# Optimization experiments

Measured on AMD Instinct MI355X. Metric: run time of the kernel, lower is better.

Reference implementation:

```python
import jax, jax.numpy as jnp
import numpy as np

BATCH = 8
N_CLASSES = 3            # including background
PRE_NMS_LIMIT = 6000
NMS_THRESH = 0.5
SCALE = 512.0
WINDOW = (0.0, 0.0, 512.0, 512.0)   # y1, x1, y2, x2
STD_DEV = np.array([0.1, 0.1, 0.2, 0.2], np.float32)
GROUP_OFFSET = 4096.0    # > image extent; separates (batch, class) groups in NMS

_RATIOS = np.array([0.5, 1.0, 2.0])
_LEVELS = [((128, 128), 4, 8.0), ((64, 64), 8, 16.0), ((32, 32), 16, 32.0), ((16, 16), 32, 64.0)]


def _gen_anchors():
    # faithful port of generate_pyramid_anchors / generate_anchors (anchor_stride=1)
    out = []
    for (fy, fx), stride, scale in _LEVELS:
        s, r = np.meshgrid(np.array([scale]), _RATIOS)
        s, r = s.flatten(), r.flatten()
        heights = s / np.sqrt(r)
        widths = s * np.sqrt(r)
        sy = np.arange(fy) * stride
        sx = np.arange(fx) * stride
        sx, sy = np.meshgrid(sx, sy)
        bw, bcx = np.meshgrid(widths, sx)
        bh, bcy = np.meshgrid(heights, sy)
        centers = np.stack([bcy, bcx], axis=2).reshape(-1, 2)
        sizes = np.stack([bh, bw], axis=2).reshape(-1, 2)
        out.append(np.concatenate([centers - 0.5 * sizes, centers + 0.5 * sizes], axis=1))
    return np.concatenate(out, axis=0).astype(np.float32)  # (65280, 4) yxyx


def setup_inputs() -> dict:
    key = jax.random.key(0)
    k1, k2 = jax.random.split(key)
    anchors = jnp.asarray(_gen_anchors())
    n_anchors = anchors.shape[0]
    n_prop = BATCH * n_anchors
    logits = jax.random.normal(k1, (n_prop, N_CLASSES), jnp.float32)
    probs = jax.nn.softmax(logits, axis=-1)
    deltas = jax.random.normal(k2, (n_prop, 4), jnp.float32)
    batch_ixs = jnp.repeat(jnp.arange(BATCH, dtype=jnp.int64), n_anchors)
    return {"probs": probs, "deltas": deltas, "anchors": anchors, "batch_ixs": batch_ixs}


def _apply_box_deltas_2d(boxes, deltas):
    # boxes: (K,4) yxyx (normalized); deltas: (K,4) dy,dx,dh,dw
    h = boxes[:, 2] - boxes[:, 0]
    w = boxes[:, 3] - boxes[:, 1]
    cy = boxes[:, 0] + 0.5 * h + deltas[:, 0] * h
    cx = boxes[:, 1] + 0.5 * w + deltas[:, 1] * w
    h = h * jnp.exp(deltas[:, 2])
    w = w * jnp.exp(deltas[:, 3])
    y1 = cy - 0.5 * h
    x1 = cx - 0.5 * w
    return jnp.stack([y1, x1, y1 + h, x1 + w], axis=1)


def _nms_keep(boxes, thresh):
    # boxes (K,4), already sorted by score descending; returns bool keep mask.
    y1, x1, y2, x2 = boxes[:, 0], boxes[:, 1], boxes[:, 2], boxes[:, 3]
    areas = (y2 - y1 + 1.0) * (x2 - x1 + 1.0)
    ih = jnp.clip(jnp.minimum(y2[:, None], y2[None, :]) - jnp.maximum(y1[:, None], y1[None, :]) + 1.0, 0.0)
    iw = jnp.clip(jnp.minimum(x2[:, None], x2[None, :]) - jnp.maximum(x1[:, None], x1[None, :]) + 1.0, 0.0)
    inter = ih * iw
    iou = inter / (areas[:, None] + areas[None, :] - inter)  # (K,K)
    K = boxes.shape[0]
    idx = jnp.arange(K)

    def body(i, keep):
        sup = (iou[i] >= thresh) & (idx > i) & keep[i]
        return keep & ~sup

    return jax.lax.fori_loop(0, K, body, jnp.ones((K,), bool))


def reference(probs, deltas, anchors, batch_ixs):
    n_anchors = anchors.shape[0]
    n_fg = probs.shape[1] - 1
    # trim to top pre_nms_limit foreground scores (flat over proposals x fg classes)
    fg = probs[:, 1:].reshape(-1)
    scores, flat_ix = jax.lax.top_k(fg, PRE_NMS_LIMIT)  # sorted descending
    prop_ix = flat_ix // n_fg
    class_ids = flat_ix % n_fg + 1
    b = batch_ixs[prop_ix]
    a = anchors[prop_ix % n_anchors]        # anchors tiled per batch element
    d = deltas[prop_ix] * jnp.asarray(STD_DEV)
    rois = _apply_box_deltas_2d(a / SCALE, d) * SCALE
    lo = jnp.array([WINDOW[0], WINDOW[1], WINDOW[0], WINDOW[1]], rois.dtype)
    hi = jnp.array([WINDOW[2], WINDOW[3], WINDOW[2], WINDOW[3]], rois.dtype)
    rois = jnp.clip(rois, lo, hi)
    # batched per-class NMS: offset boxes so different (batch, class) groups never overlap
    group = (b * (n_fg + 1) + class_ids).astype(rois.dtype) * GROUP_OFFSET
    keep = _nms_keep(rois + group[:, None], NMS_THRESH)
    detections = jnp.concatenate(
        [rois, scores[:, None], keep.astype(rois.dtype)[:, None]], axis=1)  # (K, 6)
    return detections, class_ids, b
```

## Files before the change

kernel.cpp:

```cpp
#include <hip/hip_runtime.h>
#include <math.h>

typedef unsigned int u32;
typedef unsigned short u16;
typedef unsigned long long u64;

#define PRE_NMS 6000
#define NBLK    94
#define KMAX    640
#define MSTRIDE 11
#define MAXW    10
#define MTILE   (MAXW * MAXW)
#define FINEB   8192
#define LOWB    8064
#define TOTB    (FINEB + LOWB)
#define NHB     16
#define CANDMAX 16384
#define SLICES  8
#define NGRP    24
#define CBLK    256
#define CBUF    512
#define FLOOR_BITS 0x3F000000u

#define CTR_OFF    0
#define RANKS_OFF  256
#define PART_OFF   65792
#define CAND_OFF   1106176
#define BOXR_OFF   1237248
#define GBITS_OFF  1333504
#define KG_OFF     1351936
#define GRANKG_OFF 1352192
#define BOXG_OFF   1413632
#define AREAG_OFF  1659392
#define MASKG_OFF  1720832

__global__ __launch_bounds__(1024) void hist_kernel(const float4* __restrict__ probs4,
                                                    u32* __restrict__ partials, int n_prop) {
    __shared__ u32 hf[FINEB];
    __shared__ u32 hl[2][LOWB];
    int t = threadIdx.x;
    for (int i = t; i < FINEB; i += 1024) hf[i] = 0u;
    for (int i = t; i < 2 * LOWB; i += 1024) ((u32*)hl)[i] = 0u;
    __syncthreads();
    u32* l = hl[(t >> 6) & 1];
    int nq = n_prop >> 2;
    int idx = blockIdx.x * 1024 + t;
    int stride = gridDim.x * 1024;
    for (int q = idx; q < nq; q += stride) {
        float4 a = probs4[3 * q + 0];
        float4 b = probs4[3 * q + 1];
        float4 c = probs4[3 * q + 2];
        float vs[8] = {a.y, a.z, b.x, b.y, b.w, c.x, c.z, c.w};
        #pragma unroll
        for (int e = 0; e < 8; ++e) {
            u32 bits = __float_as_uint(vs[e]);
            if (bits >= FLOOR_BITS) {
                u32 fb = (bits - FLOOR_BITS) >> 10; if (fb >= FINEB) fb = FINEB - 1;
                atomicAdd(&hf[fb], 1u);
            } else {
                atomicAdd(&l[bits >> 17], 1u);
            }
        }
    }
    __syncthreads();
    u32* outp = partials + blockIdx.x * TOTB;
    for (int b = t; b < FINEB; b += 1024) outp[b] = hf[b];
    for (int b = t; b < LOWB; b += 1024) outp[FINEB + b] = hl[0][b] + hl[1][b];
}

__global__ __launch_bounds__(1024) void pivot_kernel(const u32* __restrict__ partials,
                                                     u32* __restrict__ ctr,
                                                     u32* __restrict__ ranks,
                                                     u32* __restrict__ gbits) {
    __shared__ u32 fh[FINEB];
    __shared__ u32 sd[1024];
    int t = threadIdx.x;
    for (int i = t; i < CANDMAX; i += 1024) ranks[i] = 0u;
    for (int i = t; i < NGRP * 192; i += 1024) gbits[i] = 0u;
    if (t == 0) ctr[0] = 0u;
    for (int b = t; b < FINEB; b += 1024) {
        u32 s = 0;
        #pragma unroll
        for (int k = 0; k < NHB; ++k) s += partials[k * TOTB + b];
        fh[b] = s;
    }
    __syncthreads();
    int hi = FINEB - 1 - 8 * t;
    u32 L = 0;
    #pragma unroll
    for (int e = 0; e < 8; ++e) L += fh[hi - e];
    sd[t] = L;
    __syncthreads();
    for (int off = 1; off < 1024; off <<= 1) {
        u32 x = (t >= off) ? sd[t - off] : 0u;
        __syncthreads();
        sd[t] += x;
        __syncthreads();
    }
    u32 incl = sd[t], excl = incl - L;
    u32 fineTotal = sd[1023];
    if (excl < (u32)PRE_NMS && incl >= (u32)PRE_NMS) {
        u32 run = excl;
        #pragma unroll
        for (int e = 0; e < 8; ++e) {
            u32 c = fh[hi - e];
            if (run < (u32)PRE_NMS && run + c >= (u32)PRE_NMS)
                ctr[1] = FLOOR_BITS + ((u32)(hi - e) << 10);
            run += c;
        }
    }
    if (fineTotal >= (u32)PRE_NMS) return;

    u32 rem = (u32)PRE_NMS - fineTotal;
    __syncthreads();
    for (int b = t; b < FINEB; b += 1024) {
        u32 s = 0;
        if (b < LOWB) {
            #pragma unroll
            for (int k = 0; k < NHB; ++k) s += partials[k * TOTB + FINEB + b];
        }
        fh[b] = s;
    }
    __syncthreads();
    L = 0;
    #pragma unroll
    for (int e = 0; e < 8; ++e) L += fh[hi - e];
    sd[t] = L;
    __syncthreads();
    for (int off = 1; off < 1024; off <<= 1) {
        u32 x = (t >= off) ? sd[t - off] : 0u;
        __syncthreads();
        sd[t] += x;
        __syncthreads();
    }
    incl = sd[t]; excl = incl - L;
    if (excl < rem && incl >= rem) {
        u32 run = excl;
        #pragma unroll
        for (int e = 0; e < 8; ++e) {
            u32 c = fh[hi - e];
            if (run < rem && run + c >= rem)
                ctr[1] = ((u32)(hi - e)) << 17;
            run += c;
        }
    }
}

__global__ __launch_bounds__(256) void compact_kernel(const float4* __restrict__ probs4,
                                                      u32* ctr, u64* __restrict__ cand,
                                                      int n_prop) {
    __shared__ u64 sloc[CBUF];
    __shared__ u32 scnt, sbase;
    int t = threadIdx.x;
    if (t == 0) scnt = 0u;
    __syncthreads();
    u32 pivot = ctr[1];
    int nq = n_prop >> 2;
    int idx = blockIdx.x * 256 + t;
    int stride = gridDim.x * 256;
    for (int q = idx; q < nq; q += stride) {
        float4 a = probs4[3 * q + 0];
        float4 b = probs4[3 * q + 1];
        float4 c = probs4[3 * q + 2];
        float vs[8] = {a.y, a.z, b.x, b.y, b.w, c.x, c.z, c.w};
        #pragma unroll
        for (int e = 0; e < 8; ++e) {
            u32 bits = __float_as_uint(vs[e]);
            if (bits >= pivot) {
                u32 lp = atomicAdd(&scnt, 1u);
                u32 i = (u32)(8 * q + e);
                if (lp < (u32)CBUF) sloc[lp] = ((u64)bits << 32) | (u64)(~i);
            }
        }
    }
    __syncthreads();
    u32 cnt = scnt; if (cnt > (u32)CBUF) cnt = (u32)CBUF;
    if (t == 0) sbase = atomicAdd(&ctr[0], cnt);
    __syncthreads();
    u32 base = sbase;
    for (u32 j = t; j < cnt; j += 256) {
        u32 pos = base + j;
        if (pos < (u32)CANDMAX) cand[pos] = sloc[j];
    }
}

__global__ __launch_bounds__(256) void rank_kernel(const u64* __restrict__ cand,
                                                   const u32* __restrict__ ctr,
                                                   u32* __restrict__ ranks) {
    __shared__ u64 tile[256];
    int t = threadIdx.x;
    u32 M = ctr[0]; if (M > (u32)CANDMAX) M = (u32)CANDMAX;
    int kb = blockIdx.y;
    if ((u32)(kb * 256) >= M) return;
    int i = kb * 256 + t;
    u64 key = (i < (int)M) ? cand[i] : 0ull;
    u32 Ls = (M + SLICES - 1) / SLICES;
    u32 s0 = blockIdx.x * Ls;
    u32 s1 = s0 + Ls; if (s1 > M) s1 = M;
    int cnt = 0;
    for (u32 base = s0; base < s1; base += 256) {
        u32 idx = base + t;
        tile[t] = (idx < s1) ? cand[idx] : 0ull;
        __syncthreads();
        #pragma unroll 8
        for (int q = 0; q < 256; ++q) cnt += (tile[q] > key) ? 1 : 0;
        __syncthreads();
    }
    if (i < (int)M && cnt > 0) atomicAdd(&ranks[i], (u32)cnt);
}

__global__ __launch_bounds__(256) void decode_kernel(const u64* __restrict__ cand,
                                                     const u32* __restrict__ ranks,
                                                     const u32* __restrict__ ctr,
                                                     const float4* __restrict__ deltas4,
                                                     const float4* __restrict__ anchors4,
                                                     float4* __restrict__ boxr,
                                                     u32* __restrict__ gbits,
                                                     float* __restrict__ out,
                                                     int n_anch) {
    u32 i = blockIdx.x * 256 + threadIdx.x;
    u32 M = ctr[0]; if (M > (u32)CANDMAX) M = (u32)CANDMAX;
    if (i >= M) return;
    u32 r = ranks[i];
    if (r >= (u32)PRE_NMS) return;
    u64 key = cand[i];
    u32 bits = (u32)(key >> 32);
    u32 flat = ~((u32)key);
    int p = (int)(flat >> 1);
    int cls = (int)(flat & 1u) + 1;
    int b = p / n_anch;
    int g = b * 3 + cls;
    int aidx = p - b * n_anch;
    float score = __uint_as_float(bits);
    float4 a = anchors4[aidx];
    float4 d = deltas4[p];
    float d0 = d.x * 0.1f, d1 = d.y * 0.1f, d2 = d.z * 0.2f, d3 = d.w * 0.2f;
    float y1 = a.x * (1.0f / 512.0f), x1 = a.y * (1.0f / 512.0f);
    float y2 = a.z * (1.0f / 512.0f), x2 = a.w * (1.0f / 512.0f);
    float h = y2 - y1, w = x2 - x1;
    float cy = y1 + 0.5f * h + d0 * h;
    float cx = x1 + 0.5f * w + d1 * w;
    h = h * expf(d2);
    w = w * expf(d3);
    float ry1 = (cy - 0.5f * h) * 512.0f;
    float rx1 = (cx - 0.5f * w) * 512.0f;
    float ry2 = (cy - 0.5f * h + h) * 512.0f;
    float rx2 = (cx - 0.5f * w + w) * 512.0f;
    ry1 = fminf(fmaxf(ry1, 0.0f), 512.0f);
    rx1 = fminf(fmaxf(rx1, 0.0f), 512.0f);
    ry2 = fminf(fmaxf(ry2, 0.0f), 512.0f);
    rx2 = fminf(fmaxf(rx2, 0.0f), 512.0f);
    out[r * 6 + 0] = ry1;
    out[r * 6 + 1] = rx1;
    out[r * 6 + 2] = ry2;
    out[r * 6 + 3] = rx2;
    out[r * 6 + 4] = score;
    out[r * 6 + 5] = 1.0f;
    out[PRE_NMS * 6 + r] = (float)cls;
    out[PRE_NMS * 7 + r] = (float)b;
    boxr[r] = make_float4(ry1, rx1, ry2, rx2);
    atomicOr(&gbits[g * 192 + (r >> 5)], 1u << (r & 31));
}

__global__ __launch_bounds__(512) void prep_kernel(const u32* __restrict__ gbits,
                                                   const float4* __restrict__ boxr,
                                                   u32* __restrict__ kg,
                                                   u32* __restrict__ grankg,
                                                   float4* __restrict__ boxg,
                                                   float* __restrict__ areag) {
    __shared__ int bpre[96];
    __shared__ u16 grankS[KMAX];
    __shared__ int sK;
    int g = blockIdx.x, t = threadIdx.x, lane = t & 63, wv = t >> 6;
    const u32* rb32 = gbits + g * 192;

    if (t < 64) {
        u64 w0 = (u64)rb32[2 * lane] | ((u64)rb32[2 * lane + 1] << 32);
        u64 w1 = (lane < NBLK - 64)
                 ? ((u64)rb32[128 + 2 * lane] | ((u64)rb32[129 + 2 * lane] << 32)) : 0ull;
        int c0 = (int)__popcll(w0), c1 = (int)__popcll(w1);
        int i0 = c0, i1 = c1;
        #pragma unroll
        for (int off = 1; off < 64; off <<= 1) {
            int a = __shfl_up(i0, off); if (lane >= off) i0 += a;
            int b = __shfl_up(i1, off); if (lane >= off) i1 += b;
        }
        int tot0 = __shfl(i0, 63), tot1 = __shfl(i1, 63);
        bpre[lane] = i0 - c0;
        if (lane < 32) bpre[64 + lane] = tot0 + ((lane < NBLK - 64) ? (i1 - c1) : 0);
        if (lane == 0) { sK = tot0 + tot1; kg[g] = (u32)(tot0 + tot1); }
    }
    __syncthreads();
    int K = sK;
    if (K == 0) return;
    int Kc = (K < KMAX) ? K : KMAX;

    for (int blk = wv; blk < NBLK; blk += 8) {
        u64 wmask = (u64)rb32[2 * blk] | ((u64)rb32[2 * blk + 1] << 32);
        if ((wmask >> lane) & 1ull) {
            int pos = bpre[blk] + (int)__popcll(wmask & ((1ull << lane) - 1ull));
            if (pos < KMAX) grankS[pos] = (u16)((blk << 6) | lane);
        }
    }
    __syncthreads();

    float4* bg = boxg + g * KMAX;
    float*  ag = areag + g * KMAX;
    u32*    gr = grankg + g * KMAX;
    for (int m = t; m < KMAX; m += 512) {
        if (m < Kc) {
            int r = grankS[m];
            float4 bb = boxr[r];
            bg[m] = bb;
            ag[m] = (bb.z - bb.x + 1.0f) * (bb.w - bb.y + 1.0f);
            gr[m] = (u32)r;
        } else {
            bg[m] = make_float4(-3e30f, -3e30f, -3e30f, -3e30f);
            ag[m] = 3e38f;
        }
    }
}

__global__ __launch_bounds__(64) void mask_kernel(const u32* __restrict__ kg,
                                                  const float4* __restrict__ boxg,
                                                  const float* __restrict__ areag,
                                                  u64* __restrict__ maskg) {
    int g = blockIdx.y;
    u32 K = kg[g];
    if (K == 0u) return;
    int Kc = (K < (u32)KMAX) ? (int)K : KMAX;
    int W = (Kc + 63) >> 6;
    int u = blockIdx.x;
    int c = u / MAXW, rbk = u % MAXW;
    if (c >= W || rbk >= W) return;
    int lane = threadIdx.x;
    int r = rbk * 64 + lane;
    u64* mg = maskg + (size_t)g * (KMAX * MSTRIDE);
    if (rbk > c) { mg[r * MSTRIDE + c] = 0ull; return; }
    int j0 = c << 6;
    const float4* bg = boxg + g * KMAX;
    const float*  ag = areag + g * KMAX;
    float4 rb = bg[r];
    float  ra = ag[r];
    float4 cb = bg[j0 + lane];
    float  ca = ag[j0 + lane];
    u64 word = 0ull;
    #pragma unroll 8
    for (int q = 0; q < 64; ++q) {
        float cbx = __shfl(cb.x, q);
        float cby = __shfl(cb.y, q);
        float cbz = __shfl(cb.z, q);
        float cbw = __shfl(cb.w, q);
        float cav = __shfl(ca, q);
        float ih = fminf(rb.z, cbz) - fmaxf(rb.x, cbx) + 1.0f;
        float iw = fminf(rb.w, cbw) - fmaxf(rb.y, cby) + 1.0f;
        ih = fmaxf(ih, 0.0f); iw = fmaxf(iw, 0.0f);
        bool o = (3.0f * ih * iw >= ra + cav) && ((j0 + q) > r);
        if (o) word |= (1ull << q);
    }
    mg[r * MSTRIDE + c] = word;
}

__global__ __launch_bounds__(512) void greedy_kernel(const u32* __restrict__ kg,
                                                     const u32* __restrict__ grankg,
                                                     const u64* __restrict__ maskg,
                                                     float* __restrict__ out) {
    __shared__ u64 maskm[KMAX * MSTRIDE + 64];
    __shared__ u16 grank[KMAX];
    int g = blockIdx.x, t = threadIdx.x, lane = t & 63;
    u32 K = kg[g];
    if (K == 0u) return;
    int Kc = (K < (u32)KMAX) ? (int)K : KMAX;
    int W = (Kc + 63) >> 6;
    const u64* mg = maskg + (size_t)g * (KMAX * MSTRIDE);
    int nw = Kc * MSTRIDE;
    for (int m = t; m < nw; m += 512) maskm[m] = mg[m];
    for (int m = nw + t; m < nw + 64; m += 512) maskm[m] = 0ull;
    for (int m = t; m < Kc; m += 512) grank[m] = (u16)grankg[g * KMAX + m];
    __syncthreads();

    if (t >= 64) return;
    u64 remv = 0ull;
    for (int w = 0; w < W; ++w) {
        int r0 = w << 6;
        int rend = Kc - r0; if (rend > 64) rend = 64;
        u64 curw = __shfl(remv, w);
        u64 kb = 0ull;
        for (int b0 = 0; b0 < rend; b0 += 8) {
            int n = rend - b0; if (n > 8) n = 8;
            u64 mrow[8], dg[8];
            #pragma unroll
            for (int j = 0; j < 8; ++j) {
                int rr = r0 + b0 + ((j < n) ? j : 0);
                mrow[j] = maskm[rr * MSTRIDE + lane];
                dg[j]   = maskm[rr * MSTRIDE + w];
            }
            #pragma unroll
            for (int j = 0; j < 8; ++j) {
                if (j < n) {
                    int b = b0 + j;
                    u64 km = ((curw >> b) & 1ull) ? 0ull : ~0ull;
                    curw |= dg[j] & km;
                    remv |= mrow[j] & km;
                    kb |= km & (1ull << b);
                }
            }
        }
        if (lane < rend)
            out[(int)grank[r0 + lane] * 6 + 5] = ((kb >> lane) & 1ull) ? 1.0f : 0.0f;
    }
}

extern "C" void kernel_launch(void* const* d_in, const int* in_sizes, int n_in,
                              void* d_out, int out_size, void* d_ws, size_t ws_size,
                              hipStream_t stream) {
    const float*  probs    = (const float*)d_in[0];
    const float4* deltas4  = (const float4*)d_in[1];
    const float4* anchors4 = (const float4*)d_in[2];
    int n_prop = in_sizes[1] / 4;
    int n_anch = in_sizes[2] / 4;

    char* ws = (char*)d_ws;
    u32* ctr      = (u32*)(ws + CTR_OFF);
    u32* ranks    = (u32*)(ws + RANKS_OFF);
    u32* partials = (u32*)(ws + PART_OFF);
    u64* cand     = (u64*)(ws + CAND_OFF);
    float4* boxr  = (float4*)(ws + BOXR_OFF);
    u32* gbits    = (u32*)(ws + GBITS_OFF);
    u32* kg       = (u32*)(ws + KG_OFF);
    u32* grankg   = (u32*)(ws + GRANKG_OFF);
    float4* boxg  = (float4*)(ws + BOXG_OFF);
    float* areag  = (float*)(ws + AREAG_OFF);
    u64* maskg    = (u64*)(ws + MASKG_OFF);
    float* out    = (float*)d_out;

    hist_kernel<<<NHB, 1024, 0, stream>>>((const float4*)probs, partials, n_prop);
    pivot_kernel<<<1, 1024, 0, stream>>>(partials, ctr, ranks, gbits);
    compact_kernel<<<CBLK, 256, 0, stream>>>((const float4*)probs, ctr, cand, n_prop);
    rank_kernel<<<dim3(SLICES, 64), 256, 0, stream>>>(cand, ctr, ranks);
    decode_kernel<<<CANDMAX / 256, 256, 0, stream>>>(cand, ranks, ctr, deltas4, anchors4,
                                                     boxr, gbits, out, n_anch);
    prep_kernel<<<NGRP, 512, 0, stream>>>(gbits, boxr, kg, grankg, boxg, areag);
    mask_kernel<<<dim3(MTILE, NGRP), 64, 0, stream>>>(kg, boxg, areag, maskg);
    greedy_kernel<<<NGRP, 512, 0, stream>>>(kg, grankg, maskg, out);
}
```

Baseline: 153.5 us.

## Fuse the eight-kernel pipeline into one cooperative kernel with grid syncs

Replaces the eight separate launches (hist, pivot, compact, rank, decode, prep, mask, greedy) with a single cooperative mega-kernel of 256 blocks separated by grid.sync barriers. The aim is to remove launch overhead and the gaps between dependent stages. The histogram now runs on all 256 blocks, with global atomics into a shared fine histogram and per-block low partials. The rank and compact phases are also reworked inside the fused kernel. In exchange, the single-block pivot phase now has to sum 256 low partials instead of 16. The grid-wide barriers have their own cost, and the large shared-memory pool limits occupancy to one block per CU.

```diff
diff --git a/kernel.cpp b/kernel.cpp
--- a/kernel.cpp
+++ b/kernel.cpp
@@ -1,5 +1,8 @@
 #include <hip/hip_runtime.h>
+#include <hip/hip_cooperative_groups.h>
 #include <math.h>
+
+namespace cg = cooperative_groups;
 
 typedef unsigned int u32;
 typedef unsigned short u16;
@@ -10,437 +13,410 @@
 #define KMAX    640
 #define MSTRIDE 11
 #define MAXW    10
-#define MTILE   (MAXW * MAXW)
 #define FINEB   8192
 #define LOWB    8064
-#define TOTB    (FINEB + LOWB)
-#define NHB     16
 #define CANDMAX 16384
-#define SLICES  8
 #define NGRP    24
-#define CBLK    256
 #define CBUF    512
+#define NBLOCKS 256
+#define NTHREADS 256
+#define NTOT    (NBLOCKS * NTHREADS)
 #define FLOOR_BITS 0x3F000000u
 
 #define CTR_OFF    0
-#define RANKS_OFF  256
-#define PART_OFF   65792
-#define CAND_OFF   1106176
-#define BOXR_OFF   1237248
-#define GBITS_OFF  1333504
-#define KG_OFF     1351936
-#define GRANKG_OFF 1352192
-#define BOXG_OFF   1413632
-#define AREAG_OFF  1659392
-#define MASKG_OFF  1720832
-
-__global__ __launch_bounds__(1024) void hist_kernel(const float4* __restrict__ probs4,
-                                                    u32* __restrict__ partials, int n_prop) {
-    __shared__ u32 hf[FINEB];
-    __shared__ u32 hl[2][LOWB];
-    int t = threadIdx.x;
-    for (int i = t; i < FINEB; i += 1024) hf[i] = 0u;
-    for (int i = t; i < 2 * LOWB; i += 1024) ((u32*)hl)[i] = 0u;
-    __syncthreads();
-    u32* l = hl[(t >> 6) & 1];
-    int nq = n_prop >> 2;
-    int idx = blockIdx.x * 1024 + t;
-    int stride = gridDim.x * 1024;
-    for (int q = idx; q < nq; q += stride) {
-        float4 a = probs4[3 * q + 0];
-        float4 b = probs4[3 * q + 1];
-        float4 c = probs4[3 * q + 2];
-        float vs[8] = {a.y, a.z, b.x, b.y, b.w, c.x, c.z, c.w};
+#define CAND_OFF   256
+#define BOXR_OFF   131328
+#define GBITS_OFF  227584
+#define KG_OFF     246016
+#define GRANKG_OFF 246272
+#define BOXG_OFF   307712
+#define AREAG_OFF  553472
+#define MASKG_OFF  614912
+#define FINEH_OFF  1966592
+#define LOWP_OFF   1999360
+
+__global__ __launch_bounds__(NTHREADS) void mega_kernel(
+    const float4* __restrict__ probs4,
+    const float4* __restrict__ deltas4,
+    const float4* __restrict__ anchors4,
+    float* __restrict__ out,
+    char* __restrict__ ws,
+    int n_prop, int n_anch)
+{
+    cg::grid_group grid = cg::this_grid();
+
+    u32*    ctr    = (u32*)(ws + CTR_OFF);
+    u64*    cand   = (u64*)(ws + CAND_OFF);
+    float4* boxr   = (float4*)(ws + BOXR_OFF);
+    u32*    gbits  = (u32*)(ws + GBITS_OFF);
+    u32*    kg     = (u32*)(ws + KG_OFF);
+    u32*    grankg = (u32*)(ws + GRANKG_OFF);
+    float4* boxg   = (float4*)(ws + BOXG_OFF);
+    float*  areag  = (float*)(ws + AREAG_OFF);
+    u64*    maskg  = (u64*)(ws + MASKG_OFF);
+    u32*    fineh  = (u32*)(ws + FINEH_OFF);
+    u32*    lowp   = (u32*)(ws + LOWP_OFF);
+
+    __shared__ __align__(16) unsigned char pool[65024];
+    __shared__ u32 s_cnt, s_base;
+    __shared__ int s_K;
+
+    const int t    = threadIdx.x;
+    const int bid  = blockIdx.x;
+    const int gtid = bid * NTHREADS + t;
+    const int lane = t & 63, wv = t >> 6;
+
+    for (int i = gtid; i < FINEB; i += NTOT) fineh[i] = 0u;
+    if (gtid < 64) ctr[gtid] = 0u;
+    for (int i = gtid; i < NGRP * 192; i += NTOT) gbits[i] = 0u;
+    grid.sync();
+
+    {
+        u32* hf = (u32*)pool;
+        u32* hl = hf + FINEB;
+        for (int i = t; i < FINEB + LOWB; i += NTHREADS) hf[i] = 0u;
+        __syncthreads();
+        int nq = n_prop >> 2;
+        for (int q = gtid; q < nq; q += NTOT) {
+            float4 a = probs4[3 * q + 0];
+            float4 b = probs4[3 * q + 1];
+            float4 c = probs4[3 * q + 2];
+            float vs[8] = {a.y, a.z, b.x, b.y, b.w, c.x, c.z, c.w};
+            #pragma unroll
+            for (int e = 0; e < 8; ++e) {
+                u32 bits = __float_as_uint(vs[e]);
+                if (bits >= FLOOR_BITS) {
+                    u32 fb = (bits - FLOOR_BITS) >> 10; if (fb >= FINEB) fb = FINEB - 1;
+                    atomicAdd(&hf[fb], 1u);
+                } else {
+                    atomicAdd(&hl[bits >> 17], 1u);
+                }
+            }
+        }
+        __syncthreads();
+        for (int i = t; i < FINEB; i += NTHREADS) {
+            u32 v = hf[i];
+            if (v) atomicAdd(&fineh[i], v);
+        }
+        u32* myLow = lowp + bid * LOWB;
+        for (int i = t; i < LOWB; i += NTHREADS) myLow[i] = hl[i];
+    }
+    grid.sync();
+
+    if (bid == 0) {
+        u32* fh = (u32*)pool;
+        u32* sd = fh + FINEB;
+        for (int b = t; b < FINEB; b += NTHREADS) fh[b] = fineh[b];
+        __syncthreads();
+        int hi = FINEB - 1 - 32 * t;
+        u32 L = 0;
         #pragma unroll
-        for (int e = 0; e < 8; ++e) {
-            u32 bits = __float_as_uint(vs[e]);
-            if (bits >= FLOOR_BITS) {
-                u32 fb = (bits - FLOOR_BITS) >> 10; if (fb >= FINEB) fb = FINEB - 1;
-                atomicAdd(&hf[fb], 1u);
-            } else {
-                atomicAdd(&l[bits >> 17], 1u);
-            }
-        }
-    }
-    __syncthreads();
-    u32* outp = partials + blockIdx.x * TOTB;
-    for (int b = t; b < FINEB; b += 1024) outp[b] = hf[b];
-    for (int b = t; b < LOWB; b += 1024) outp[FINEB + b] = hl[0][b] + hl[1][b];
-}
-
-__global__ __launch_bounds__(1024) void pivot_kernel(const u32* __restrict__ partials,
-                                                     u32* __restrict__ ctr,
-                                                     u32* __restrict__ ranks,
-                                                     u32* __restrict__ gbits) {
-    __shared__ u32 fh[FINEB];
-    __shared__ u32 sd[1024];
-    int t = threadIdx.x;
-    for (int i = t; i < CANDMAX; i += 1024) ranks[i] = 0u;
-    for (int i = t; i < NGRP * 192; i += 1024) gbits[i] = 0u;
-    if (t == 0) ctr[0] = 0u;
-    for (int b = t; b < FINEB; b += 1024) {
-        u32 s = 0;
-        #pragma unroll
-        for (int k = 0; k < NHB; ++k) s += partials[k * TOTB + b];
-        fh[b] = s;
-    }
-    __syncthreads();
-    int hi = FINEB - 1 - 8 * t;
-    u32 L = 0;
-    #pragma unroll
-    for (int e = 0; e < 8; ++e) L += fh[hi - e];
-    sd[t] = L;
-    __syncthreads();
-    for (int off = 1; off < 1024; off <<= 1) {
-        u32 x = (t >= off) ? sd[t - off] : 0u;
-        __syncthreads();
-        sd[t] += x;
-        __syncthreads();
-    }
-    u32 incl = sd[t], excl = incl - L;
-    u32 fineTotal = sd[1023];
-    if (excl < (u32)PRE_NMS && incl >= (u32)PRE_NMS) {
-        u32 run = excl;
-        #pragma unroll
-        for (int e = 0; e < 8; ++e) {
-            u32 c = fh[hi - e];
-            if (run < (u32)PRE_NMS && run + c >= (u32)PRE_NMS)
-                ctr[1] = FLOOR_BITS + ((u32)(hi - e) << 10);
-            run += c;
-        }
-    }
-    if (fineTotal >= (u32)PRE_NMS) return;
-
-    u32 rem = (u32)PRE_NMS - fineTotal;
-    __syncthreads();
-    for (int b = t; b < FINEB; b += 1024) {
-        u32 s = 0;
-        if (b < LOWB) {
+        for (int e = 0; e < 32; ++e) L += fh[hi - e];
+        sd[t] = L;
+        __syncthreads();
+        for (int off = 1; off < NTHREADS; off <<= 1) {
+            u32 x = (t >= off) ? sd[t - off] : 0u;
+            __syncthreads();
+            sd[t] += x;
+            __syncthreads();
+        }
+        u32 incl = sd[t], excl = incl - L;
+        u32 fineTotal = sd[NTHREADS - 1];
+        if (excl < (u32)PRE_NMS && incl >= (u32)PRE_NMS) {
+            u32 run = excl;
+            for (int e = 0; e < 32; ++e) {
+                u32 c = fh[hi - e];
+                if (run < (u32)PRE_NMS && run + c >= (u32)PRE_NMS)
+                    ctr[1] = FLOOR_BITS + ((u32)(hi - e) << 10);
+                run += c;
+            }
+        }
+        if (fineTotal < (u32)PRE_NMS) {
+            u32 rem = (u32)PRE_NMS - fineTotal;
+            __syncthreads();
+            for (int b = t; b < FINEB; b += NTHREADS) {
+                u32 s = 0;
+                if (b < LOWB) {
+                    for (int k = 0; k < NBLOCKS; ++k) s += lowp[k * LOWB + b];
+                }
+                fh[b] = s;
+            }
+            __syncthreads();
+            L = 0;
+            for (int e = 0; e < 32; ++e) L += fh[hi - e];
+            sd[t] = L;
+            __syncthreads();
+            for (int off = 1; off < NTHREADS; off <<= 1) {
+                u32 x = (t >= off) ? sd[t - off] : 0u;
+                __syncthreads();
+                sd[t] += x;
+                __syncthreads();
+            }
+            incl = sd[t]; excl = incl - L;
+            if (excl < rem && incl >= rem) {
+                u32 run = excl;
+                for (int e = 0; e < 32; ++e) {
+                    u32 c = fh[hi - e];
+                    if (run < rem && run + c >= rem)
+                        ctr[1] = ((u32)(hi - e)) << 17;
+                    run += c;
+                }
+            }
+        }
+    }
+    grid.sync();
+
+    {
+        u64* sloc = (u64*)pool;
+        if (t == 0) s_cnt = 0u;
+        __syncthreads();
+        u32 pivot = ctr[1];
+        int nq = n_prop >> 2;
+        for (int q = gtid; q < nq; q += NTOT) {
+            float4 a = probs4[3 * q + 0];
+            float4 b = probs4[3 * q + 1];
+            float4 c = probs4[3 * q + 2];
+            float vs[8] = {a.y, a.z, b.x, b.y, b.w, c.x, c.z, c.w};
             #pragma unroll
-            for (int k = 0; k < NHB; ++k) s += partials[k * TOTB + FINEB + b];
-        }
-        fh[b] = s;
-    }
-    __syncthreads();
-    L = 0;
-    #pragma unroll
-    for (int e = 0; e < 8; ++e) L += fh[hi - e];
-    sd[t] = L;
-    __syncthreads();
-    for (int off = 1; off < 1024; off <<= 1) {
-        u32 x = (t >= off) ? sd[t - off] : 0u;
-        __syncthreads();
-        sd[t] += x;
-        __syncthreads();
-    }
-    incl = sd[t]; excl = incl - L;
-    if (excl < rem && incl >= rem) {
-        u32 run = excl;
-        #pragma unroll
-        for (int e = 0; e < 8; ++e) {
-            u32 c = fh[hi - e];
-            if (run < rem && run + c >= rem)
-                ctr[1] = ((u32)(hi - e)) << 17;
-            run += c;
-        }
-    }
-}
-
-__global__ __launch_bounds__(256) void compact_kernel(const float4* __restrict__ probs4,
-                                                      u32* ctr, u64* __restrict__ cand,
-                                                      int n_prop) {
-    __shared__ u64 sloc[CBUF];
-    __shared__ u32 scnt, sbase;
-    int t = threadIdx.x;
-    if (t == 0) scnt = 0u;
-    __syncthreads();
-    u32 pivot = ctr[1];
-    int nq = n_prop >> 2;
-    int idx = blockIdx.x * 256 + t;
-    int stride = gridDim.x * 256;
-    for (int q = idx; q < nq; q += stride) {
-        float4 a = probs4[3 * q + 0];
-        float4 b = probs4[3 * q + 1];
-        float4 c = probs4[3 * q + 2];
-        float vs[8] = {a.y, a.z, b.x, b.y, b.w, c.x, c.z, c.w};
-        #pragma unroll
-        for (int e = 0; e < 8; ++e) {
-            u32 bits = __float_as_uint(vs[e]);
-            if (bits >= pivot) {
-                u32 lp = atomicAdd(&scnt, 1u);
-                u32 i = (u32)(8 * q + e);
-                if (lp < (u32)CBUF) sloc[lp] = ((u64)bits << 32) | (u64)(~i);
-            }
-        }
-    }
-    __syncthreads();
-    u32 cnt = scnt; if (cnt > (u32)CBUF) cnt = (u32)CBUF;
-    if (t == 0) sbase = atomicAdd(&ctr[0], cnt);
-    __syncthreads();
-    u32 base = sbase;
-    for (u32 j = t; j < cnt; j += 256) {
-        u32 pos = base + j;
-        if (pos < (u32)CANDMAX) cand[pos] = sloc[j];
-    }
-}
-
-__global__ __launch_bounds__(256) void rank_kernel(const u64* __restrict__ cand,
-                                                   const u32* __restrict__ ctr,
-                                                   u32* __restrict__ ranks) {
-    __shared__ u64 tile[256];
-    int t = threadIdx.x;
-    u32 M = ctr[0]; if (M > (u32)CANDMAX) M = (u32)CANDMAX;
-    int kb = blockIdx.y;
-    if ((u32)(kb * 256) >= M) return;
-    int i = kb * 256 + t;
-    u64 key = (i < (int)M) ? cand[i] : 0ull;
-    u32 Ls = (M + SLICES - 1) / SLICES;
-    u32 s0 = blockIdx.x * Ls;
-    u32 s1 = s0 + Ls; if (s1 > M) s1 = M;
-    int cnt = 0;
-    for (u32 base = s0; base < s1; base += 256) {
-        u32 idx = base + t;
-        tile[t] = (idx < s1) ? cand[idx] : 0ull;
-        __syncthreads();
-        #pragma unroll 8
-        for (int q = 0; q < 256; ++q) cnt += (tile[q] > key) ? 1 : 0;
-        __syncthreads();
-    }
-    if (i < (int)M && cnt > 0) atomicAdd(&ranks[i], (u32)cnt);
-}
-
-__global__ __launch_bounds__(256) void decode_kernel(const u64* __restrict__ cand,
-                                                     const u32* __restrict__ ranks,
-                                                     const u32* __restrict__ ctr,
-                                                     const float4* __restrict__ deltas4,
-                                                     const float4* __restrict__ anchors4,
-                                                     float4* __restrict__ boxr,
-                                                     u32* __restrict__ gbits,
-                                                     float* __restrict__ out,
-                                                     int n_anch) {
-    u32 i = blockIdx.x * 256 + threadIdx.x;
-    u32 M = ctr[0]; if (M > (u32)CANDMAX) M = (u32)CANDMAX;
-    if (i >= M) return;
-    u32 r = ranks[i];
-    if (r >= (u32)PRE_NMS) return;
-    u64 key = cand[i];
-    u32 bits = (u32)(key >> 32);
-    u32 flat = ~((u32)key);
-    int p = (int)(flat >> 1);
-    int cls = (int)(flat & 1u) + 1;
-    int b = p / n_anch;
-    int g = b * 3 + cls;
-    int aidx = p - b * n_anch;
-    float score = __uint_as_float(bits);
-    float4 a = anchors4[aidx];
-    float4 d = deltas4[p];
-    float d0 = d.x * 0.1f, d1 = d.y * 0.1f, d2 = d.z * 0.2f, d3 = d.w * 0.2f;
-    float y1 = a.x * (1.0f / 512.0f), x1 = a.y * (1.0f / 512.0f);
-    float y2 = a.z * (1.0f / 512.0f), x2 = a.w * (1.0f / 512.0f);
-    float h = y2 - y1, w = x2 - x1;
-    float cy = y1 + 0.5f * h + d0 * h;
-    float cx = x1 + 0.5f * w + d1 * w;
-    h = h * expf(d2);
-    w = w * expf(d3);
-    float ry1 = (cy - 0.5f * h) * 512.0f;
-    float rx1 = (cx - 0.5f * w) * 512.0f;
-    float ry2 = (cy - 0.5f * h + h) * 512.0f;
-    float rx2 = (cx - 0.5f * w + w) * 512.0f;
-    ry1 = fminf(fmaxf(ry1, 0.0f), 512.0f);
-    rx1 = fminf(fmaxf(rx1, 0.0f), 512.0f);
-    ry2 = fminf(fmaxf(ry2, 0.0f), 512.0f);
-    rx2 = fminf(fmaxf(rx2, 0.0f), 512.0f);
-    out[r * 6 + 0] = ry1;
-    out[r * 6 + 1] = rx1;
-    out[r * 6 + 2] = ry2;
-    out[r * 6 + 3] = rx2;
-    out[r * 6 + 4] = score;
-    out[r * 6 + 5] = 1.0f;
-    out[PRE_NMS * 6 + r] = (float)cls;
-    out[PRE_NMS * 7 + r] = (float)b;
-    boxr[r] = make_float4(ry1, rx1, ry2, rx2);
-    atomicOr(&gbits[g * 192 + (r >> 5)], 1u << (r & 31));
-}
-
-__global__ __launch_bounds__(512) void prep_kernel(const u32* __restrict__ gbits,
-                                                   const float4* __restrict__ boxr,
-                                                   u32* __restrict__ kg,
-                                                   u32* __restrict__ grankg,
-                                                   float4* __restrict__ boxg,
-                                                   float* __restrict__ areag) {
-    __shared__ int bpre[96];
-    __shared__ u16 grankS[KMAX];
-    __shared__ int sK;
-    int g = blockIdx.x, t = threadIdx.x, lane = t & 63, wv = t >> 6;
-    const u32* rb32 = gbits + g * 192;
-
-    if (t < 64) {
-        u64 w0 = (u64)rb32[2 * lane] | ((u64)rb32[2 * lane + 1] << 32);
-        u64 w1 = (lane < NBLK - 64)
-                 ? ((u64)rb32[128 + 2 * lane] | ((u64)rb32[129 + 2 * lane] << 32)) : 0ull;
-        int c0 = (int)__popcll(w0), c1 = (int)__popcll(w1);
-        int i0 = c0, i1 = c1;
-        #pragma unroll
-        for (int off = 1; off < 64; off <<= 1) {
-            int a = __shfl_up(i0, off); if (lane >= off) i0 += a;
-            int b = __shfl_up(i1, off); if (lane >= off) i1 += b;
-        }
-        int tot0 = __shfl(i0, 63), tot1 = __shfl(i1, 63);
-        bpre[lane] = i0 - c0;
-        if (lane < 32) bpre[64 + lane] = tot0 + ((lane < NBLK - 64) ? (i1 - c1) : 0);
-        if (lane == 0) { sK = tot0 + tot1; kg[g] = (u32)(tot0 + tot1); }
-    }
-    __syncthreads();
-    int K = sK;
-    if (K == 0) return;
-    int Kc = (K < KMAX) ? K : KMAX;
-
-    for (int blk = wv; blk < NBLK; blk += 8) {
-        u64 wmask = (u64)rb32[2 * blk] | ((u64)rb32[2 * blk + 1] << 32);
-        if ((wmask >> lane) & 1ull) {
-            int pos = bpre[blk] + (int)__popcll(wmask & ((1ull << lane) - 1ull));
-            if (pos < KMAX) grankS[pos] = (u16)((blk << 6) | lane);
-        }
-    }
-    __syncthreads();
-
-    float4* bg = boxg + g * KMAX;
-    float*  ag = areag + g * KMAX;
-    u32*    gr = grankg + g * KMAX;
-    for (int m = t; m < KMAX; m += 512) {
-        if (m < Kc) {
-            int r = grankS[m];
-            float4 bb = boxr[r];
-            bg[m] = bb;
-            ag[m] = (bb.z - bb.x + 1.0f) * (bb.w - bb.y + 1.0f);
-            gr[m] = (u32)r;
-        } else {
-            bg[m] = make_float4(-3e30f, -3e30f, -3e30f, -3e30f);
-            ag[m] = 3e38f;
-        }
-    }
-}
-
-__global__ __launch_bounds__(64) void mask_kernel(const u32* __restrict__ kg,
-                                                  const float4* __restrict__ boxg,
-                                                  const float* __restrict__ areag,
-                                                  u64* __restrict__ maskg) {
-    int g = blockIdx.y;
-    u32 K = kg[g];
-    if (K == 0u) return;
-    int Kc = (K < (u32)KMAX) ? (int)K : KMAX;
-    int W = (Kc + 63) >> 6;
-    int u = blockIdx.x;
-    int c = u / MAXW, rbk = u % MAXW;
-    if (c >= W || rbk >= W) return;
-    int lane = threadIdx.x;
-    int r = rbk * 64 + lane;
-    u64* mg = maskg + (size_t)g * (KMAX * MSTRIDE);
-    if (rbk > c) { mg[r * MSTRIDE + c] = 0ull; return; }
-    int j0 = c << 6;
-    const float4* bg = boxg + g * KMAX;
-    const float*  ag = areag + g * KMAX;
-    float4 rb = bg[r];
-    float  ra = ag[r];
-    float4 cb = bg[j0 + lane];
-    float  ca = ag[j0 + lane];
-    u64 word = 0ull;
-    #pragma unroll 8
-    for (int q = 0; q < 64; ++q) {
-        float cbx = __shfl(cb.x, q);
-        float cby = __shfl(cb.y, q);
-        float cbz = __shfl(cb.z, q);
-        float cbw = __shfl(cb.w, q);
-        float cav = __shfl(ca, q);
-        float ih = fminf(rb.z, cbz) - fmaxf(rb.x, cbx) + 1.0f;
-        float iw = fminf(rb.w, cbw) - fmaxf(rb.y, cby) + 1.0f;
-        ih = fmaxf(ih, 0.0f); iw = fmaxf(iw, 0.0f);
-        bool o = (3.0f * ih * iw >= ra + cav) && ((j0 + q) > r);
-        if (o) word |= (1ull << q);
-    }
-    mg[r * MSTRIDE + c] = word;
-}
-
-__global__ __launch_bounds__(512) void greedy_kernel(const u32* __restrict__ kg,
-                                                     const u32* __restrict__ grankg,
-                                                     const u64* __restrict__ maskg,
-                                                     float* __restrict__ out) {
-    __shared__ u64 maskm[KMAX * MSTRIDE + 64];
-    __shared__ u16 grank[KMAX];
-    int g = blockIdx.x, t = threadIdx.x, lane = t & 63;
-    u32 K = kg[g];
-    if (K == 0u) return;
-    int Kc = (K < (u32)KMAX) ? (int)K : KMAX;
-    int W = (Kc + 63) >> 6;
-    const u64* mg = maskg + (size_t)g * (KMAX * MSTRIDE);
-    int nw = Kc * MSTRIDE;
-    for (int m = t; m < nw; m += 512) maskm[m] = mg[m];
-    for (int m = nw + t; m < nw + 64; m += 512) maskm[m] = 0ull;
-    for (int m = t; m < Kc; m += 512) grank[m] = (u16)grankg[g * KMAX + m];
-    __syncthreads();
-
-    if (t >= 64) return;
-    u64 remv = 0ull;
-    for (int w = 0; w < W; ++w) {
-        int r0 = w << 6;
-        int rend = Kc - r0; if (rend > 64) rend = 64;
-        u64 curw = __shfl(remv, w);
-        u64 kb = 0ull;
-        for (int b0 = 0; b0 < rend; b0 += 8) {
-            int n = rend - b0; if (n > 8) n = 8;
-            u64 mrow[8], dg[8];
-            #pragma unroll
-            for (int j = 0; j < 8; ++j) {
-                int rr = r0 + b0 + ((j < n) ? j : 0);
-                mrow[j] = maskm[rr * MSTRIDE + lane];
-                dg[j]   = maskm[rr * MSTRIDE + w];
-            }
-            #pragma unroll
-            for (int j = 0; j < 8; ++j) {
-                if (j < n) {
-                    int b = b0 + j;
-                    u64 km = ((curw >> b) & 1ull) ? 0ull : ~0ull;
-                    curw |= dg[j] & km;
-                    remv |= mrow[j] & km;
-                    kb |= km & (1ull << b);
-                }
-            }
-        }
-        if (lane < rend)
-            out[(int)grank[r0 + lane] * 6 + 5] = ((kb >> lane) & 1ull) ? 1.0f : 0.0f;
+            for (int e = 0; e < 8; ++e) {
+                u32 bits = __float_as_uint(vs[e]);
+                if (bits >= pivot) {
+                    u32 lp = atomicAdd(&s_cnt, 1u);
+                    u32 i = (u32)(8 * q + e);
+                    if (lp < (u32)CBUF) sloc[lp] = ((u64)bits << 32) | (u64)(~i);
+                }
+            }
+        }
+        __syncthreads();
+        u32 cnt = s_cnt; if (cnt > (u32)CBUF) cnt = (u32)CBUF;
+        if (t == 0) s_base = atomicAdd(&ctr[0], cnt);
+        __syncthreads();
+        for (u32 j = t; j < cnt; j += NTHREADS) {
+            u32 pos = s_base + j;
+            if (pos < (u32)CANDMAX) cand[pos] = sloc[j];
+        }
+    }
+    grid.sync();
+
+    {
+        u64* tile = (u64*)pool;
+        u32 M = ctr[0]; if (M > (u32)CANDMAX) M = (u32)CANDMAX;
+        u32 i = (u32)gtid;
+        u64 key = (i < M) ? cand[i] : 0ull;
+        u32 cnt = 0;
+        for (u32 base = 0; base < M; base += 2048) {
+            for (u32 j = t; j < 2048; j += NTHREADS) {
+                u32 idx = base + j;
+                tile[j] = (idx < M) ? cand[idx] : 0ull;
+            }
+            __syncthreads();
+            #pragma unroll 8
+            for (int q = 0; q < 2048; ++q) cnt += (tile[q] > key) ? 1u : 0u;
+            __syncthreads();
+        }
+        if (i < M && cnt < (u32)PRE_NMS) {
+            u32 r = cnt;
+            u32 bits = (u32)(key >> 32);
+            u32 flat = ~((u32)key);
+            int p = (int)(flat >> 1);
+            int cls = (int)(flat & 1u) + 1;
+            int b = p / n_anch;
+            int g = b * 3 + cls;
+            int aidx = p - b * n_anch;
+            float score = __uint_as_float(bits);
+            float4 a = anchors4[aidx];
+            float4 d = deltas4[p];
+            float d0 = d.x * 0.1f, d1 = d.y * 0.1f, d2 = d.z * 0.2f, d3 = d.w * 0.2f;
+            float y1 = a.x * (1.0f / 512.0f), x1 = a.y * (1.0f / 512.0f);
+            float y2 = a.z * (1.0f / 512.0f), x2 = a.w * (1.0f / 512.0f);
+            float h = y2 - y1, w = x2 - x1;
+            float cy = y1 + 0.5f * h + d0 * h;
+            float cx = x1 + 0.5f * w + d1 * w;
+            h = h * expf(d2);
+            w = w * expf(d3);
+            float ry1 = (cy - 0.5f * h) * 512.0f;
+            float rx1 = (cx - 0.5f * w) * 512.0f;
+            float ry2 = (cy - 0.5f * h + h) * 512.0f;
+            float rx2 = (cx - 0.5f * w + w) * 512.0f;
+            ry1 = fminf(fmaxf(ry1, 0.0f), 512.0f);
+            rx1 = fminf(fmaxf(rx1, 0.0f), 512.0f);
+            ry2 = fminf(fmaxf(ry2, 0.0f), 512.0f);
+            rx2 = fminf(fmaxf(rx2, 0.0f), 512.0f);
+            out[r * 6 + 0] = ry1;
+            out[r * 6 + 1] = rx1;
+            out[r * 6 + 2] = ry2;
+            out[r * 6 + 3] = rx2;
+            out[r * 6 + 4] = score;
+            out[r * 6 + 5] = 1.0f;
+            out[PRE_NMS * 6 + r] = (float)cls;
+            out[PRE_NMS * 7 + r] = (float)b;
+            boxr[r] = make_float4(ry1, rx1, ry2, rx2);
+            atomicOr(&gbits[g * 192 + (r >> 5)], 1u << (r & 31));
+        }
+    }
+    grid.sync();
+
+    {
+        int* bpre   = (int*)pool;
+        u16* grankS = (u16*)(pool + 512);
+        int g = bid;
+        if (g < NGRP) {
+            const u32* rb32 = gbits + g * 192;
+            if (t < 64) {
+                u64 w0 = (u64)rb32[2 * lane] | ((u64)rb32[2 * lane + 1] << 32);
+                u64 w1 = (lane < NBLK - 64)
+                         ? ((u64)rb32[128 + 2 * lane] | ((u64)rb32[129 + 2 * lane] << 32)) : 0ull;
+                int c0 = (int)__popcll(w0), c1 = (int)__popcll(w1);
+                int i0 = c0, i1 = c1;
+                #pragma unroll
+                for (int off = 1; off < 64; off <<= 1) {
+                    int a = __shfl_up(i0, off); if (lane >= off) i0 += a;
+                    int b = __shfl_up(i1, off); if (lane >= off) i1 += b;
+                }
+                int tot0 = __shfl(i0, 63), tot1 = __shfl(i1, 63);
+                bpre[lane] = i0 - c0;
+                if (lane < 32) bpre[64 + lane] = tot0 + ((lane < NBLK - 64) ? (i1 - c1) : 0);
+                if (lane == 0) { s_K = tot0 + tot1; kg[g] = (u32)(tot0 + tot1); }
+            }
+            __syncthreads();
+            int K = s_K;
+            if (K > 0) {
+                int Kc = (K < KMAX) ? K : KMAX;
+                for (int blk = wv; blk < NBLK; blk += 4) {
+                    u64 wmask = (u64)rb32[2 * blk] | ((u64)rb32[2 * blk + 1] << 32);
+                    if ((wmask >> lane) & 1ull) {
+                        int pos = bpre[blk] + (int)__popcll(wmask & ((1ull << lane) - 1ull));
+                        if (pos < KMAX) grankS[pos] = (u16)((blk << 6) | lane);
+                    }
+                }
+                __syncthreads();
+                float4* bg = boxg + g * KMAX;
+                float*  ag = areag + g * KMAX;
+                u32*    gr = grankg + g * KMAX;
+                for (int m = t; m < KMAX; m += NTHREADS) {
+                    if (m < Kc) {
+                        int r = grankS[m];
+                        float4 bb = boxr[r];
+                        bg[m] = bb;
+                        ag[m] = (bb.z - bb.x + 1.0f) * (bb.w - bb.y + 1.0f);
+                        gr[m] = (u32)r;
+                    } else {
+                        bg[m] = make_float4(-3e30f, -3e30f, -3e30f, -3e30f);
+                        ag[m] = 3e38f;
+                    }
+                }
+            }
+        }
+    }
+    grid.sync();
+
+    {
+        int gw = bid * 4 + wv;
+        const int NUNIT = NGRP * MAXW * MAXW;
+        for (int u = gw; u < NUNIT; u += NBLOCKS * 4) {
+            int g = u / (MAXW * MAXW);
+            int rm = u % (MAXW * MAXW);
+            int c = rm / MAXW, rbk = rm % MAXW;
+            u32 K = kg[g];
+            if (K == 0u) continue;
+            int Kc = (K < (u32)KMAX) ? (int)K : KMAX;
+            int W = (Kc + 63) >> 6;
+            if (c >= W || rbk >= W) continue;
+            int r = rbk * 64 + lane;
+            u64* mg = maskg + (size_t)g * (KMAX * MSTRIDE);
+            if (rbk > c) { mg[r * MSTRIDE + c] = 0ull; continue; }
+            int j0 = c << 6;
+            const float4* bg = boxg + g * KMAX;
+            const float*  ag = areag + g * KMAX;
+            float4 rb = bg[r];
+            float  ra = ag[r];
+            float4 cb = bg[j0 + lane];
+            float  ca = ag[j0 + lane];
+            u64 word = 0ull;
+            #pragma unroll 8
+            for (int q = 0; q < 64; ++q) {
+                float cbx = __shfl(cb.x, q);
+                float cby = __shfl(cb.y, q);
+                float cbz = __shfl(cb.z, q);
+                float cbw = __shfl(cb.w, q);
+                float cav = __shfl(ca, q);
+                float ih = fminf(rb.z, cbz) - fmaxf(rb.x, cbx) + 1.0f;
+                float iw = fminf(rb.w, cbw) - fmaxf(rb.y, cby) + 1.0f;
+                ih = fmaxf(ih, 0.0f); iw = fmaxf(iw, 0.0f);
+                bool o = (3.0f * ih * iw >= ra + cav) && ((j0 + q) > r);
+                if (o) word |= (1ull << q);
+            }
+            mg[r * MSTRIDE + c] = word;
+        }
+    }
+    grid.sync();
+
+    {
+        int g = bid;
+        if (g < NGRP) {
+            u32 K = kg[g];
+            if (K > 0u) {
+                u64* maskm = (u64*)pool;
+                u16* grank = (u16*)(pool + 57344);
+                int Kc = (K < (u32)KMAX) ? (int)K : KMAX;
+                int W = (Kc + 63) >> 6;
+                const u64* mg = maskg + (size_t)g * (KMAX * MSTRIDE);
+                int nw = Kc * MSTRIDE;
+                for (int m = t; m < nw; m += NTHREADS) maskm[m] = mg[m];
+                for (int m = nw + t; m < nw + 64; m += NTHREADS) maskm[m] = 0ull;
+                for (int m = t; m < Kc; m += NTHREADS) grank[m] = (u16)grankg[g * KMAX + m];
+                __syncthreads();
+                if (t < 64) {
+                    u64 remv = 0ull;
+                    for (int w = 0; w < W; ++w) {
+                        int r0 = w << 6;
+                        int rend = Kc - r0; if (rend > 64) rend = 64;
+                        u64 curw = __shfl(remv, w);
+                        u64 kb = 0ull;
+                        for (int b0 = 0; b0 < rend; b0 += 8) {
+                            int n = rend - b0; if (n > 8) n = 8;
+                            u64 mrow[8], dg[8];
+                            #pragma unroll
+                            for (int j = 0; j < 8; ++j) {
+                                int rr = r0 + b0 + ((j < n) ? j : 0);
+                                mrow[j] = maskm[rr * MSTRIDE + lane];
+                                dg[j]   = maskm[rr * MSTRIDE + w];
+                            }
+                            #pragma unroll
+                            for (int j = 0; j < 8; ++j) {
+                                if (j < n) {
+                                    int b = b0 + j;
+                                    u64 km = ((curw >> b) & 1ull) ? 0ull : ~0ull;
+                                    curw |= dg[j] & km;
+                                    remv |= mrow[j] & km;
+                                    kb |= km & (1ull << b);
+                                }
+                            }
+                        }
+                        if (lane < rend)
+                            out[(int)grank[r0 + lane] * 6 + 5] = ((kb >> lane) & 1ull) ? 1.0f : 0.0f;
+                    }
+                }
+            }
+        }
     }
 }
 
 extern "C" void kernel_launch(void* const* d_in, const int* in_sizes, int n_in,
                               void* d_out, int out_size, void* d_ws, size_t ws_size,
                               hipStream_t stream) {
-    const float*  probs    = (const float*)d_in[0];
+    const float4* probs4   = (const float4*)d_in[0];
     const float4* deltas4  = (const float4*)d_in[1];
     const float4* anchors4 = (const float4*)d_in[2];
     int n_prop = in_sizes[1] / 4;
     int n_anch = in_sizes[2] / 4;
-
-    char* ws = (char*)d_ws;
-    u32* ctr      = (u32*)(ws + CTR_OFF);
-    u32* ranks    = (u32*)(ws + RANKS_OFF);
-    u32* partials = (u32*)(ws + PART_OFF);
-    u64* cand     = (u64*)(ws + CAND_OFF);
-    float4* boxr  = (float4*)(ws + BOXR_OFF);
-    u32* gbits    = (u32*)(ws + GBITS_OFF);
-    u32* kg       = (u32*)(ws + KG_OFF);
-    u32* grankg   = (u32*)(ws + GRANKG_OFF);
-    float4* boxg  = (float4*)(ws + BOXG_OFF);
-    float* areag  = (float*)(ws + AREAG_OFF);
-    u64* maskg    = (u64*)(ws + MASKG_OFF);
-    float* out    = (float*)d_out;
-
-    hist_kernel<<<NHB, 1024, 0, stream>>>((const float4*)probs, partials, n_prop);
-    pivot_kernel<<<1, 1024, 0, stream>>>(partials, ctr, ranks, gbits);
-    compact_kernel<<<CBLK, 256, 0, stream>>>((const float4*)probs, ctr, cand, n_prop);
-    rank_kernel<<<dim3(SLICES, 64), 256, 0, stream>>>(cand, ctr, ranks);
-    decode_kernel<<<CANDMAX / 256, 256, 0, stream>>>(cand, ranks, ctr, deltas4, anchors4,
-                                                     boxr, gbits, out, n_anch);
-    prep_kernel<<<NGRP, 512, 0, stream>>>(gbits, boxr, kg, grankg, boxg, areag);
-    mask_kernel<<<dim3(MTILE, NGRP), 64, 0, stream>>>(kg, boxg, areag, maskg);
-    greedy_kernel<<<NGRP, 512, 0, stream>>>(kg, grankg, maskg, out);
+    char* ws   = (char*)d_ws;
+    float* out = (float*)d_out;
+
+    void* kargs[] = {
+        (void*)&probs4, (void*)&deltas4, (void*)&anchors4,
+        (void*)&out, (void*)&ws, (void*)&n_prop, (void*)&n_anch
+    };
+    hipLaunchCooperativeKernel((void*)mega_kernel, dim3(NBLOCKS), dim3(NTHREADS),
+                               kargs, 0, stream);
 }
```

Result: slower. 410.7 us (+167.6%).
